# Optimization experiments

Measured on AMD Instinct MI355X. Metric: run time of the kernel, lower is better.

## Reference

```python
import jax, jax.numpy as jnp
import numpy as np

N_PARTICLES = 3_000_000
N_CVS = 30_000
N_MODELS = 8
FEATS = [64, 64, 64, 64]
E0, E1 = 2.0, 3.0
LN_EPS = 1e-5


def _dihedral(p):
    # p: [4,3] -> scalar dihedral angle (standard atan2 formulation)
    b1 = p[1] - p[0]
    b2 = p[2] - p[1]
    b3 = p[3] - p[2]
    n1 = jnp.cross(b1, b2)
    n2 = jnp.cross(b2, b3)
    m1 = jnp.cross(n1, b2 / jnp.linalg.norm(b2))
    return jnp.arctan2(jnp.dot(m1, n2), jnp.dot(n1, n2))


def _ensemble_energy(cvs, gamma, beta, Ws, bs):
    # cvs: [n_cvs] -> energy per model: [n_models]
    x = jnp.concatenate([jnp.cos(cvs), jnp.sin(cvs)])  # [2*n_cvs]
    mu = jnp.mean(x)
    var = jnp.mean((x - mu) ** 2)
    x = (x - mu) / jnp.sqrt(var + LN_EPS) * gamma + beta  # LayerNorm
    h = x[None, None, :]  # [1,1,2n] broadcasts against [M,2n,f]
    for i in range(len(Ws) - 1):
        h = jax.nn.relu(jnp.matmul(h, Ws[i]) + bs[i])  # [M,1,f]
    h = jnp.matmul(h, Ws[-1]) + bs[-1]  # [M,1,1]
    return h[:, 0, 0]  # [M]  (squeeze(-1) then batch dim 1)


def _uncertainty_weight(model_div):
    iswitch = (E1 - model_div) / (E1 - E0)
    fl = jnp.floor(iswitch)
    smooth = 0.5 * (1.0 + jnp.cos(jnp.pi * (1.0 - iswitch)))
    # heaviside(floor(iswitch), smooth): 1 if floor>0, smooth if floor==0, 0 if floor<0
    return jnp.where(fl > 0, 1.0, jnp.where(fl < 0, 0.0, smooth)).astype(model_div.dtype)


def setup_inputs() -> dict:
    key = jax.random.key(0)
    ks = jax.random.split(key, 16)
    positions = jax.random.normal(ks[0], (N_PARTICLES, 3), jnp.float32) * 3.0
    boxvectors = jnp.diag(jnp.full((3,), 10.0, dtype=jnp.float32))
    colvar_idx = jax.random.randint(ks[1], (N_CVS, 4), 0, N_PARTICLES)
    dims = [2 * N_CVS] + FEATS + [1]
    inp = {"positions": positions, "boxvectors": boxvectors, "colvar_idx": colvar_idx,
           "gamma": jnp.ones((2 * N_CVS,), jnp.float32),
           "beta": jnp.zeros((2 * N_CVS,), jnp.float32)}
    for i in range(5):
        bound = 1.0 / np.sqrt(dims[i])  # kaiming_uniform-like bound
        inp[f"W{i}"] = jax.random.uniform(ks[2 + i], (N_MODELS, dims[i], dims[i + 1]),
                                           jnp.float32, -bound, bound)
        inp[f"b{i}"] = jnp.zeros((N_MODELS, 1, dims[i + 1]), jnp.float32)
    return inp


def reference(positions, boxvectors, colvar_idx, gamma, beta,
              W0, b0, W1, b1, W2, b2, W3, b3, W4, b4):
    Ws = [W0, W1, W2, W3, W4]
    bs = [b0, b1, b2, b3, b4]
    boxsize = jnp.diag(boxvectors)  # [3]
    pos = positions - jnp.floor(positions / boxsize) * boxsize  # PBC wrap
    quads = pos[colvar_idx.reshape(-1)].reshape(-1, 4, 3)  # [n_cvs,4,3]
    cvs, dcvs_dx = jax.vmap(jax.value_and_grad(_dihedral))(quads)  # [n],[n,4,3]

    efn = lambda c: _ensemble_energy(c, gamma, beta, Ws, bs)  # [M]
    energy = efn(cvs)  # [M]
    mean_forces = -jax.jacrev(efn)(cvs)  # [M, n_cvs]: grad of -energy[m] wrt cvs

    model_div = jnp.sqrt(jnp.mean(jnp.var(mean_forces, axis=0, ddof=1)))
    sigma = _uncertainty_weight(model_div)
    mf = jnp.mean(mean_forces, axis=0)  # [n_cvs]
    contrib = (mf[:, None, None] * dcvs_dx).reshape(-1, 3)  # [n_cvs*4,3]
    forces = jnp.zeros_like(pos).at[colvar_idx.reshape(-1)].add(contrib)
    return energy.mean() * sigma, forces * sigma
```

## Files before the change

kernel.cpp:

```cpp
#include <hip/hip_runtime.h>
#include <math.h>

#define NCV   30000
#define NX    60000
#define NM    8
#define LN_EPSF 1e-5f
#define NFORCE 9000000

#define NB_CV 512
#define JB    59
#define NBX   235
#define NB_MF 118

#define WS_XRAW   0
#define WS_DCV    60000
#define WS_G      420000
#define WS_LNP    900000
#define WS_Z0P    901024
#define WS_DZ0    931232
#define WS_E      931744
#define WS_SGP    931752
#define WS_SGXP   933632
#define WS_VARSUM 935512
#define WS_TICKET 935513
#define WS_SIGMA  935514
#define WS_FLAG   935515

struct F3 { float x, y, z; };
__device__ __forceinline__ F3 f3sub(F3 a, F3 b){ return {a.x-b.x, a.y-b.y, a.z-b.z}; }
__device__ __forceinline__ F3 f3add(F3 a, F3 b){ return {a.x+b.x, a.y+b.y, a.z+b.z}; }
__device__ __forceinline__ F3 f3scale(F3 a, float s){ return {a.x*s, a.y*s, a.z*s}; }
__device__ __forceinline__ float f3dot(F3 a, F3 b){ return a.x*b.x + a.y*b.y + a.z*b.z; }
__device__ __forceinline__ F3 f3cross(F3 a, F3 b){
  return { a.y*b.z - a.z*b.y, a.z*b.x - a.x*b.z, a.x*b.y - a.y*b.x };
}

__device__ __forceinline__ void compute_mu_inv(const float* __restrict__ ws, float* out2, int tid) {
  if (tid < 64) {
    float a = 0.f, b = 0.f;
    #pragma unroll 4
    for (int k = tid; k < NB_CV; k += 64) { a += ws[WS_LNP + k]; b += ws[WS_LNP + NB_CV + k]; }
    #pragma unroll
    for (int o = 1; o < 64; o <<= 1) { a += __shfl_xor(a, o); b += __shfl_xor(b, o); }
    if (tid == 0) {
      float mu  = a * (1.f / NX);
      float var = b * (1.f / NX) - mu * mu;
      out2[0] = mu;
      out2[1] = 1.f / sqrtf(var + LN_EPSF);
    }
  }
}

__global__ void k_cv(const float* __restrict__ pos, const float* __restrict__ box,
                     const int* __restrict__ idx, float* __restrict__ ws) {
  int tid = threadIdx.x;
  int gtid = blockIdx.x * 256 + tid;
  if (gtid == 0) {
    ws[WS_VARSUM] = 0.f;
    ((unsigned int*)ws)[WS_TICKET] = 0u;
    ((unsigned int*)ws)[WS_FLAG]   = 0u;
  }

  float cx = 0.f, cx2 = 0.f;
  int i = gtid;
  if (i < NCV) {
    float bx = box[0], by = box[4], bz = box[8];
    int4 q4 = *(const int4*)(idx + i*4);
    int pidx[4] = {q4.x, q4.y, q4.z, q4.w};
    F3 p[4];
    #pragma unroll
    for (int a = 0; a < 4; a++) {
      int pi = pidx[a];
      float X = pos[(size_t)pi*3 + 0];
      float Y = pos[(size_t)pi*3 + 1];
      float Z = pos[(size_t)pi*3 + 2];
      X -= floorf(X / bx) * bx;
      Y -= floorf(Y / by) * by;
      Z -= floorf(Z / bz) * bz;
      p[a] = {X, Y, Z};
    }
    F3 b1 = f3sub(p[1], p[0]);
    F3 b2 = f3sub(p[2], p[1]);
    F3 b3 = f3sub(p[3], p[2]);
    F3 n1 = f3cross(b1, b2);
    F3 n2 = f3cross(b2, b3);
    float L = sqrtf(f3dot(b2, b2));
    F3 u = f3scale(b2, 1.f / L);
    F3 m1 = f3cross(n1, u);
    float yv = f3dot(m1, n2);
    float xv = f3dot(n1, n2);
    float h = sqrtf(xv*xv + yv*yv);
    float cphi = xv / h;
    float sphi = yv / h;

    float invd = 1.f / (h*h);
    float dX = -yv * invd;
    float dY =  xv * invd;
    F3 dn1 = f3scale(n2, dX);
    F3 dn2 = f3scale(n1, dX);
    F3 dm1 = f3scale(n2, dY);
    dn2 = f3add(dn2, f3scale(m1, dY));
    dn1 = f3add(dn1, f3cross(u, dm1));
    F3 du = f3cross(dm1, n1);
    float ud = f3dot(u, du);
    F3 db2 = f3scale(f3sub(du, f3scale(u, ud)), 1.f / L);
    db2 = f3add(db2, f3cross(b3, dn2));
    F3 db3 = f3cross(dn2, b2);
    F3 db1 = f3cross(b2, dn1);
    db2 = f3add(db2, f3cross(dn1, b1));

    F3 g0 = f3scale(db1, -1.f);
    F3 g1 = f3sub(db1, db2);
    F3 g2 = f3sub(db2, db3);
    F3 g3 = db3;

    ws[WS_XRAW + i]       = cphi;
    ws[WS_XRAW + NCV + i] = sphi;
    float* dc = ws + WS_DCV + (size_t)i * 12;
    dc[0] = g0.x; dc[1]  = g0.y; dc[2]  = g0.z;
    dc[3] = g1.x; dc[4]  = g1.y; dc[5]  = g1.z;
    dc[6] = g2.x; dc[7]  = g2.y; dc[8]  = g2.z;
    dc[9] = g3.x; dc[10] = g3.y; dc[11] = g3.z;

    cx  = cphi + sphi;
    cx2 = cphi*cphi + sphi*sphi;
  }

  #pragma unroll
  for (int o = 1; o < 64; o <<= 1) { cx += __shfl_xor(cx, o); cx2 += __shfl_xor(cx2, o); }
  __shared__ float sa[4], sb[4];
  int w = tid >> 6, l = tid & 63;
  if (l == 0) { sa[w] = cx; sb[w] = cx2; }
  __syncthreads();
  if (tid == 0) {
    ws[WS_LNP + blockIdx.x]         = sa[0] + sa[1] + sa[2] + sa[3];
    ws[WS_LNP + NB_CV + blockIdx.x] = sb[0] + sb[1] + sb[2] + sb[3];
  }
}

__global__ void k_z0(const float4* __restrict__ W0, const float* __restrict__ gamma,
                     const float* __restrict__ beta, float* __restrict__ ws,
                     float* __restrict__ out) {
  __shared__ float stats[2];
  __shared__ float yl[1024];
  __shared__ float red[4][16][4];
  int tid = threadIdx.x;
  int jb = blockIdx.x, m = blockIdx.y;
  int j0 = jb * 1024;
  int jcount = min(1024, NX - j0);

  {
    int gtid = (m * JB + jb) * 256 + tid;
    float4 z4 = {0.f, 0.f, 0.f, 0.f};
    float4* fz = (float4*)(out + 4);
    const int NF4 = (NFORCE - 4) / 4;
    for (int i = gtid; i < NF4; i += JB * NM * 256) fz[i] = z4;
    if (gtid == 0) { out[1] = 0.f; out[2] = 0.f; out[3] = 0.f; out[NFORCE] = 0.f; }
  }

  compute_mu_inv(ws, stats, tid);
  __syncthreads();
  float mu = stats[0], inv = stats[1];
  for (int jj = tid; jj < 1024; jj += 256) {
    int gj = j0 + jj;
    yl[jj] = (gj < NX) ? ((ws[WS_XRAW + gj] - mu) * inv * gamma[gj] + beta[gj]) : 0.f;
  }
  __syncthreads();

  int k4 = tid & 15;
  int r  = tid >> 4;
  const float4* Wm = W0 + (size_t)m * NX * 16;
  float4 acc = {0.f, 0.f, 0.f, 0.f};
  #pragma unroll 4
  for (int j = r; j < jcount; j += 16) {
    float y = yl[j];
    float4 wv = Wm[(size_t)(j0 + j) * 16 + k4];
    acc.x += y * wv.x; acc.y += y * wv.y; acc.z += y * wv.z; acc.w += y * wv.w;
  }
  #pragma unroll
  for (int o = 16; o <= 32; o <<= 1) {
    acc.x += __shfl_xor(acc.x, o); acc.y += __shfl_xor(acc.y, o);
    acc.z += __shfl_xor(acc.z, o); acc.w += __shfl_xor(acc.w, o);
  }
  int w = tid >> 6, l = tid & 63;
  if (l < 16) {
    red[w][l][0] = acc.x; red[w][l][1] = acc.y; red[w][l][2] = acc.z; red[w][l][3] = acc.w;
  }
  __syncthreads();
  if (tid < 64) {
    int kk4 = tid & 15, c = tid >> 4;
    float v = red[0][kk4][c] + red[1][kk4][c] + red[2][kk4][c] + red[3][kk4][c];
    ws[WS_Z0P + ((size_t)m * JB + jb) * 64 + kk4 * 4 + c] = v;
  }
}

__global__ void k_mlp(const float* __restrict__ ws_ro, const float* __restrict__ b0,
                      const float* __restrict__ W1, const float* __restrict__ b1,
                      const float* __restrict__ W2, const float* __restrict__ b2,
                      const float* __restrict__ W3, const float* __restrict__ b3,
                      const float* __restrict__ W4, const float* __restrict__ b4,
                      float* __restrict__ ws) {
  int m = blockIdx.x;
  int tid = threadIdx.x;
  int k = tid & 63, q = tid >> 6;
  __shared__ float Wl[3][64*65];
  __shared__ float hs[4][64];
  __shared__ float part[256];
  __shared__ float ds[64];

  const float* Wsrc0 = W1 + m*4096;
  const float* Wsrc1 = W2 + m*4096;
  const float* Wsrc2 = W3 + m*4096;
  for (int e = tid; e < 4096; e += 256) {
    int t = e >> 6, kk = e & 63;
    Wl[0][t*65 + kk] = Wsrc0[e];
    Wl[1][t*65 + kk] = Wsrc1[e];
    Wl[2][t*65 + kk] = Wsrc2[e];
  }

  float p0 = 0.f;
  for (int jb = q; jb < JB; jb += 4)
    p0 += ws_ro[WS_Z0P + ((size_t)m * JB + jb) * 64 + k];
  part[tid] = p0;
  __syncthreads();
  if (tid < 64) {
    float a0 = b0[m*64 + k] + part[k] + part[64+k] + part[128+k] + part[192+k];
    hs[0][k] = fmaxf(a0, 0.f);
  }
  __syncthreads();

  #pragma unroll
  for (int l = 0; l < 3; l++) {
    float pp = 0.f;
    #pragma unroll
    for (int t0 = 0; t0 < 16; t0++) {
      int t = q*16 + t0;
      pp += hs[l][t] * Wl[l][t*65 + k];
    }
    part[tid] = pp;
    __syncthreads();
    if (tid < 64) {
      const float* bl = (l==0) ? b1 : (l==1) ? b2 : b3;
      float a = bl[m*64+k] + part[k] + part[64+k] + part[128+k] + part[192+k];
      hs[l+1][k] = fmaxf(a, 0.f);
    }
    __syncthreads();
  }

  if (tid < 64) {
    float w4k = W4[m*64 + k];
    float e = hs[3][k] * w4k;
    #pragma unroll
    for (int o = 1; o < 64; o <<= 1) e += __shfl_xor(e, o);
    if (k == 0) ws[WS_E + m] = e + b4[m];
    ds[k] = (hs[3][k] > 0.f) ? w4k : 0.f;
  }
  __syncthreads();

  #pragma unroll
  for (int l = 2; l >= 0; l--) {
    float pp = 0.f;
    int t = k;
    #pragma unroll
    for (int k0 = 0; k0 < 16; k0++) {
      int kk = q*16 + k0;
      pp += Wl[l][t*65 + kk] * ds[kk];
    }
    part[tid] = pp;
    __syncthreads();
    if (tid < 64) {
      float dh = part[k] + part[64+k] + part[128+k] + part[192+k];
      float dz = (hs[l][k] > 0.f) ? dh : 0.f;
      if (l == 0) ws[WS_DZ0 + m*64 + k] = dz;
      else        ds[k] = dz;
    }
    __syncthreads();
  }
}

__global__ void k_bwdx(const float4* __restrict__ W0, const float* __restrict__ gamma,
                       float* __restrict__ ws) {
  __shared__ float stats[2];
  __shared__ float dz[64];
  __shared__ float sa[4], sb[4];
  int tid = threadIdx.x;
  int m = blockIdx.y, blk = blockIdx.x;

  compute_mu_inv(ws, stats, tid);
  if (tid >= 64 && tid < 128) dz[tid - 64] = ws[WS_DZ0 + m*64 + (tid - 64)];
  __syncthreads();
  float mu = stats[0], inv = stats[1];

  int c = tid & 15;
  int g = tid >> 4;
  const float4* dz4 = (const float4*)dz;
  float4 d4 = dz4[c];

  float sg = 0.f, sgx = 0.f;
  #pragma unroll 2
  for (int it = 0; it < 16; it++) {
    int j = blk * 256 + it * 16 + g;
    if (j < NX) {
      float4 wv = W0[((size_t)m * NX + j) * 16 + c];
      float dot = wv.x*d4.x + wv.y*d4.y + wv.z*d4.z + wv.w*d4.w;
      #pragma unroll
      for (int o = 1; o < 16; o <<= 1) dot += __shfl_xor(dot, o);
      if (c == 0) {
        float gg = dot * gamma[j];
        ws[WS_G + (size_t)m * NX + j] = gg;
        float xh = (ws[WS_XRAW + j] - mu) * inv;
        sg += gg; sgx += gg * xh;
      }
    }
  }
  #pragma unroll
  for (int o = 1; o < 64; o <<= 1) { sg += __shfl_xor(sg, o); sgx += __shfl_xor(sgx, o); }
  int w = tid >> 6, l = tid & 63;
  if (l == 0) { sa[w] = sg; sb[w] = sgx; }
  __syncthreads();
  if (tid == 0) {
    ws[WS_SGP  + m * NBX + blk] = sa[0] + sa[1] + sa[2] + sa[3];
    ws[WS_SGXP + m * NBX + blk] = sb[0] + sb[1] + sb[2] + sb[3];
  }
}

__global__ void k_mf(const int* __restrict__ idx, float* __restrict__ ws,
                     float* __restrict__ out) {
  __shared__ float stats[2];
  __shared__ float sSg[NM], sSgx[NM];
  __shared__ float sv[4];
  __shared__ float ssig;
  int tid = threadIdx.x;
  int w = tid >> 6, l = tid & 63;

  compute_mu_inv(ws, stats, tid);
  for (int m = w; m < NM; m += 4) {
    float a = 0.f, b = 0.f;
    #pragma unroll 2
    for (int bb = l; bb < NBX; bb += 64) { a += ws[WS_SGP + m*NBX + bb]; b += ws[WS_SGXP + m*NBX + bb]; }
    #pragma unroll
    for (int o = 1; o < 64; o <<= 1) { a += __shfl_xor(a, o); b += __shfl_xor(b, o); }
    if (l == 0) { sSg[m] = a * (1.f / NX); sSgx[m] = b * (1.f / NX); }
  }
  __syncthreads();
  float mu = stats[0], inv = stats[1];

  int i = blockIdx.x * 256 + tid;
  float v = 0.f, fm = 0.f;
  if (i < NCV) {
    float cph = ws[WS_XRAW + i], sph = ws[WS_XRAW + NCV + i];
    float xc = (cph - mu) * inv, xs = (sph - mu) * inv;
    float f[NM];
    #pragma unroll
    for (int m = 0; m < NM; m++) {
      float gc = ws[WS_G + (size_t)m * NX + i];
      float gs = ws[WS_G + (size_t)m * NX + NCV + i];
      float dxc = inv * (gc - sSg[m] - xc * sSgx[m]);
      float dxs = inv * (gs - sSg[m] - xs * sSgx[m]);
      float dE = dxc * (-sph) + dxs * cph;
      f[m] = -dE;
      fm += f[m];
    }
    fm *= (1.f / NM);
    float acc = 0.f;
    #pragma unroll
    for (int m = 0; m < NM; m++) { float d = f[m] - fm; acc += d * d; }
    v = acc * (1.f / (NM - 1));
  }
  #pragma unroll
  for (int o = 1; o < 64; o <<= 1) v += __shfl_xor(v, o);
  if (l == 0) sv[w] = v;
  __syncthreads();
  if (tid == 0) {
    atomicAdd(&ws[WS_VARSUM], sv[0] + sv[1] + sv[2] + sv[3]);
    __threadfence();
    unsigned int* tick = (unsigned int*)ws + WS_TICKET;
    unsigned int old = atomicAdd(tick, 1u);
    if (old == NB_MF - 1) {
      float tot = atomicAdd(&ws[WS_VARSUM], 0.0f);
      float md = sqrtf(tot * (1.f / NCV));
      float isw = (3.0f - md) / (3.0f - 2.0f);
      float fl = floorf(isw);
      float smooth = 0.5f * (1.f + cosf(3.14159265358979323846f * (1.f - isw)));
      float sigma = (fl > 0.f) ? 1.f : ((fl < 0.f) ? 0.f : smooth);
      float em = 0.f;
      #pragma unroll
      for (int m = 0; m < NM; m++) em += ws[WS_E + m];
      em *= (1.f / NM);
      out[0] = em * sigma;
      __hip_atomic_store(ws + WS_SIGMA, sigma, __ATOMIC_RELAXED, __HIP_MEMORY_SCOPE_AGENT);
      __hip_atomic_store((unsigned int*)ws + WS_FLAG, 1u, __ATOMIC_RELEASE, __HIP_MEMORY_SCOPE_AGENT);
    }
    while (__hip_atomic_load((unsigned int*)ws + WS_FLAG, __ATOMIC_ACQUIRE,
                             __HIP_MEMORY_SCOPE_AGENT) == 0u) {
      __builtin_amdgcn_s_sleep(8);
    }
    ssig = __hip_atomic_load(ws + WS_SIGMA, __ATOMIC_RELAXED, __HIP_MEMORY_SCOPE_AGENT);
  }
  __syncthreads();
  float sigma = ssig;

  if (i < NCV) {
    const float* dc = ws + WS_DCV + (size_t)i * 12;
    float4 d0 = *(const float4*)(dc);
    float4 d1 = *(const float4*)(dc + 4);
    float4 d2 = *(const float4*)(dc + 8);
    int4 q4 = *(const int4*)(idx + i*4);
    float s = fm * sigma;
    float* fp = out + 1;
    atomicAdd(&fp[(size_t)q4.x*3 + 0], s*d0.x);
    atomicAdd(&fp[(size_t)q4.x*3 + 1], s*d0.y);
    atomicAdd(&fp[(size_t)q4.x*3 + 2], s*d0.z);
    atomicAdd(&fp[(size_t)q4.y*3 + 0], s*d0.w);
    atomicAdd(&fp[(size_t)q4.y*3 + 1], s*d1.x);
    atomicAdd(&fp[(size_t)q4.y*3 + 2], s*d1.y);
    atomicAdd(&fp[(size_t)q4.z*3 + 0], s*d1.z);
    atomicAdd(&fp[(size_t)q4.z*3 + 1], s*d1.w);
    atomicAdd(&fp[(size_t)q4.z*3 + 2], s*d2.x);
    atomicAdd(&fp[(size_t)q4.w*3 + 0], s*d2.y);
    atomicAdd(&fp[(size_t)q4.w*3 + 1], s*d2.z);
    atomicAdd(&fp[(size_t)q4.w*3 + 2], s*d2.w);
  }
}

extern "C" void kernel_launch(void* const* d_in, const int* in_sizes, int n_in,
                              void* d_out, int out_size, void* d_ws, size_t ws_size,
                              hipStream_t stream) {
  const float* pos   = (const float*)d_in[0];
  const float* box   = (const float*)d_in[1];
  const int*   idx   = (const int*)  d_in[2];
  const float* gamma = (const float*)d_in[3];
  const float* beta  = (const float*)d_in[4];
  const float* W0 = (const float*)d_in[5];
  const float* b0 = (const float*)d_in[6];
  const float* W1 = (const float*)d_in[7];
  const float* b1 = (const float*)d_in[8];
  const float* W2 = (const float*)d_in[9];
  const float* b2 = (const float*)d_in[10];
  const float* W3 = (const float*)d_in[11];
  const float* b3 = (const float*)d_in[12];
  const float* W4 = (const float*)d_in[13];
  const float* b4 = (const float*)d_in[14];
  float* ws  = (float*)d_ws;
  float* out = (float*)d_out;

  k_cv<<<NB_CV, 256, 0, stream>>>(pos, box, idx, ws);
  k_z0<<<dim3(JB, NM), 256, 0, stream>>>((const float4*)W0, gamma, beta, ws, out);
  k_mlp<<<NM, 256, 0, stream>>>(ws, b0, W1, b1, W2, b2, W3, b3, W4, b4, ws);
  k_bwdx<<<dim3(NBX, NM), 256, 0, stream>>>((const float4*)W0, gamma, ws);
  k_mf<<<NB_MF, 256, 0, stream>>>(idx, ws, out);
}
```

Before: 100.7 us.

## Split W0 projection into finer blocks, move force zeroing, use SoA gradients

Shrinks each k_z0 block to 128 rows so the W0 projection runs on many more blocks. The force-buffer zeroing moves from k_z0 into k_cv. The dihedral gradient storage changes to a structure-of-arrays layout for coalesced stores and loads. k_bwdx batches four W0 loads before the reductions to raise memory-level parallelism. In exchange, k_mlp must reduce eight times more partial sums, and k_cv now carries the large zeroing write.

```diff
diff --git a/kernel.cpp b/kernel.cpp
--- a/kernel.cpp
+++ b/kernel.cpp
@@ -8,7 +8,7 @@
 #define NFORCE 9000000
 
 #define NB_CV 512
-#define JB    59
+#define JB    469
 #define NBX   235
 #define NB_MF 118
 
@@ -17,14 +17,14 @@
 #define WS_G      420000
 #define WS_LNP    900000
 #define WS_Z0P    901024
-#define WS_DZ0    931232
-#define WS_E      931744
-#define WS_SGP    931752
-#define WS_SGXP   933632
-#define WS_VARSUM 935512
-#define WS_TICKET 935513
-#define WS_SIGMA  935514
-#define WS_FLAG   935515
+#define WS_DZ0    1141152
+#define WS_E      1141664
+#define WS_SGP    1141672
+#define WS_SGXP   1143552
+#define WS_VARSUM 1145432
+#define WS_TICKET 1145433
+#define WS_SIGMA  1145434
+#define WS_FLAG   1145435
 
 struct F3 { float x, y, z; };
 __device__ __forceinline__ F3 f3sub(F3 a, F3 b){ return {a.x-b.x, a.y-b.y, a.z-b.z}; }
@@ -52,13 +52,22 @@
 }
 
 __global__ void k_cv(const float* __restrict__ pos, const float* __restrict__ box,
-                     const int* __restrict__ idx, float* __restrict__ ws) {
+                     const int* __restrict__ idx, float* __restrict__ ws,
+                     float* __restrict__ out) {
   int tid = threadIdx.x;
   int gtid = blockIdx.x * 256 + tid;
-  if (gtid == 0) {
-    ws[WS_VARSUM] = 0.f;
-    ((unsigned int*)ws)[WS_TICKET] = 0u;
-    ((unsigned int*)ws)[WS_FLAG]   = 0u;
+
+  {
+    float4 z4 = {0.f, 0.f, 0.f, 0.f};
+    float4* fz = (float4*)(out + 4);
+    const int NF4 = (NFORCE - 4) / 4;
+    for (int i = gtid; i < NF4; i += NB_CV * 256) fz[i] = z4;
+    if (gtid == 0) {
+      out[1] = 0.f; out[2] = 0.f; out[3] = 0.f; out[NFORCE] = 0.f;
+      ws[WS_VARSUM] = 0.f;
+      ((unsigned int*)ws)[WS_TICKET] = 0u;
+      ((unsigned int*)ws)[WS_FLAG]   = 0u;
+    }
   }
 
   float cx = 0.f, cx2 = 0.f;
@@ -116,11 +125,10 @@
 
     ws[WS_XRAW + i]       = cphi;
     ws[WS_XRAW + NCV + i] = sphi;
-    float* dc = ws + WS_DCV + (size_t)i * 12;
-    dc[0] = g0.x; dc[1]  = g0.y; dc[2]  = g0.z;
-    dc[3] = g1.x; dc[4]  = g1.y; dc[5]  = g1.z;
-    dc[6] = g2.x; dc[7]  = g2.y; dc[8]  = g2.z;
-    dc[9] = g3.x; dc[10] = g3.y; dc[11] = g3.z;
+    ws[WS_DCV + 0*NCV  + i] = g0.x; ws[WS_DCV + 1*NCV  + i] = g0.y; ws[WS_DCV + 2*NCV  + i] = g0.z;
+    ws[WS_DCV + 3*NCV  + i] = g1.x; ws[WS_DCV + 4*NCV  + i] = g1.y; ws[WS_DCV + 5*NCV  + i] = g1.z;
+    ws[WS_DCV + 6*NCV  + i] = g2.x; ws[WS_DCV + 7*NCV  + i] = g2.y; ws[WS_DCV + 8*NCV  + i] = g2.z;
+    ws[WS_DCV + 9*NCV  + i] = g3.x; ws[WS_DCV + 10*NCV + i] = g3.y; ws[WS_DCV + 11*NCV + i] = g3.z;
 
     cx  = cphi + sphi;
     cx2 = cphi*cphi + sphi*sphi;
@@ -139,31 +147,21 @@
 }
 
 __global__ void k_z0(const float4* __restrict__ W0, const float* __restrict__ gamma,
-                     const float* __restrict__ beta, float* __restrict__ ws,
-                     float* __restrict__ out) {
+                     const float* __restrict__ beta, float* __restrict__ ws) {
   __shared__ float stats[2];
-  __shared__ float yl[1024];
+  __shared__ float yl[128];
   __shared__ float red[4][16][4];
   int tid = threadIdx.x;
   int jb = blockIdx.x, m = blockIdx.y;
-  int j0 = jb * 1024;
-  int jcount = min(1024, NX - j0);
-
-  {
-    int gtid = (m * JB + jb) * 256 + tid;
-    float4 z4 = {0.f, 0.f, 0.f, 0.f};
-    float4* fz = (float4*)(out + 4);
-    const int NF4 = (NFORCE - 4) / 4;
-    for (int i = gtid; i < NF4; i += JB * NM * 256) fz[i] = z4;
-    if (gtid == 0) { out[1] = 0.f; out[2] = 0.f; out[3] = 0.f; out[NFORCE] = 0.f; }
-  }
+  int j0 = jb * 128;
+  int jcount = min(128, NX - j0);
 
   compute_mu_inv(ws, stats, tid);
   __syncthreads();
   float mu = stats[0], inv = stats[1];
-  for (int jj = tid; jj < 1024; jj += 256) {
-    int gj = j0 + jj;
-    yl[jj] = (gj < NX) ? ((ws[WS_XRAW + gj] - mu) * inv * gamma[gj] + beta[gj]) : 0.f;
+  if (tid < 128) {
+    int gj = j0 + tid;
+    yl[tid] = (gj < NX) ? ((ws[WS_XRAW + gj] - mu) * inv * gamma[gj] + beta[gj]) : 0.f;
   }
   __syncthreads();
 
@@ -171,11 +169,14 @@
   int r  = tid >> 4;
   const float4* Wm = W0 + (size_t)m * NX * 16;
   float4 acc = {0.f, 0.f, 0.f, 0.f};
-  #pragma unroll 4
-  for (int j = r; j < jcount; j += 16) {
-    float y = yl[j];
-    float4 wv = Wm[(size_t)(j0 + j) * 16 + k4];
-    acc.x += y * wv.x; acc.y += y * wv.y; acc.z += y * wv.z; acc.w += y * wv.w;
+  #pragma unroll
+  for (int it = 0; it < 8; it++) {
+    int j = it * 16 + r;
+    if (j < jcount) {
+      float y = yl[j];
+      float4 wv = Wm[(size_t)(j0 + j) * 16 + k4];
+      acc.x += y * wv.x; acc.y += y * wv.y; acc.z += y * wv.z; acc.w += y * wv.w;
+    }
   }
   #pragma unroll
   for (int o = 16; o <= 32; o <<= 1) {
@@ -297,15 +298,23 @@
   float4 d4 = dz4[c];
 
   float sg = 0.f, sgx = 0.f;
-  #pragma unroll 2
-  for (int it = 0; it < 16; it++) {
-    int j = blk * 256 + it * 16 + g;
-    if (j < NX) {
-      float4 wv = W0[((size_t)m * NX + j) * 16 + c];
-      float dot = wv.x*d4.x + wv.y*d4.y + wv.z*d4.z + wv.w*d4.w;
+  #pragma unroll
+  for (int it = 0; it < 4; it++) {
+    int jbase = blk * 256 + it * 64 + g;
+    float4 wv[4];
+    #pragma unroll
+    for (int u = 0; u < 4; u++) {
+      int j = jbase + u * 16;
+      if (j < NX) wv[u] = W0[((size_t)m * NX + j) * 16 + c];
+      else        wv[u] = {0.f, 0.f, 0.f, 0.f};
+    }
+    #pragma unroll
+    for (int u = 0; u < 4; u++) {
+      int j = jbase + u * 16;
+      float dot = wv[u].x*d4.x + wv[u].y*d4.y + wv[u].z*d4.z + wv[u].w*d4.w;
       #pragma unroll
       for (int o = 1; o < 16; o <<= 1) dot += __shfl_xor(dot, o);
-      if (c == 0) {
+      if (c == 0 && j < NX) {
         float gg = dot * gamma[j];
         ws[WS_G + (size_t)m * NX + j] = gg;
         float xh = (ws[WS_XRAW + j] - mu) * inv;
@@ -401,25 +410,24 @@
   float sigma = ssig;
 
   if (i < NCV) {
-    const float* dc = ws + WS_DCV + (size_t)i * 12;
-    float4 d0 = *(const float4*)(dc);
-    float4 d1 = *(const float4*)(dc + 4);
-    float4 d2 = *(const float4*)(dc + 8);
+    float d[12];
+    #pragma unroll
+    for (int r = 0; r < 12; r++) d[r] = ws[WS_DCV + r*NCV + i];
     int4 q4 = *(const int4*)(idx + i*4);
     float s = fm * sigma;
     float* fp = out + 1;
-    atomicAdd(&fp[(size_t)q4.x*3 + 0], s*d0.x);
-    atomicAdd(&fp[(size_t)q4.x*3 + 1], s*d0.y);
-    atomicAdd(&fp[(size_t)q4.x*3 + 2], s*d0.z);
-    atomicAdd(&fp[(size_t)q4.y*3 + 0], s*d0.w);
-    atomicAdd(&fp[(size_t)q4.y*3 + 1], s*d1.x);
-    atomicAdd(&fp[(size_t)q4.y*3 + 2], s*d1.y);
-    atomicAdd(&fp[(size_t)q4.z*3 + 0], s*d1.z);
-    atomicAdd(&fp[(size_t)q4.z*3 + 1], s*d1.w);
-    atomicAdd(&fp[(size_t)q4.z*3 + 2], s*d2.x);
-    atomicAdd(&fp[(size_t)q4.w*3 + 0], s*d2.y);
-    atomicAdd(&fp[(size_t)q4.w*3 + 1], s*d2.z);
-    atomicAdd(&fp[(size_t)q4.w*3 + 2], s*d2.w);
+    atomicAdd(&fp[(size_t)q4.x*3 + 0], s*d[0]);
+    atomicAdd(&fp[(size_t)q4.x*3 + 1], s*d[1]);
+    atomicAdd(&fp[(size_t)q4.x*3 + 2], s*d[2]);
+    atomicAdd(&fp[(size_t)q4.y*3 + 0], s*d[3]);
+    atomicAdd(&fp[(size_t)q4.y*3 + 1], s*d[4]);
+    atomicAdd(&fp[(size_t)q4.y*3 + 2], s*d[5]);
+    atomicAdd(&fp[(size_t)q4.z*3 + 0], s*d[6]);
+    atomicAdd(&fp[(size_t)q4.z*3 + 1], s*d[7]);
+    atomicAdd(&fp[(size_t)q4.z*3 + 2], s*d[8]);
+    atomicAdd(&fp[(size_t)q4.w*3 + 0], s*d[9]);
+    atomicAdd(&fp[(size_t)q4.w*3 + 1], s*d[10]);
+    atomicAdd(&fp[(size_t)q4.w*3 + 2], s*d[11]);
   }
 }
 
@@ -444,8 +452,8 @@
   float* ws  = (float*)d_ws;
   float* out = (float*)d_out;
 
-  k_cv<<<NB_CV, 256, 0, stream>>>(pos, box, idx, ws);
-  k_z0<<<dim3(JB, NM), 256, 0, stream>>>((const float4*)W0, gamma, beta, ws, out);
+  k_cv<<<NB_CV, 256, 0, stream>>>(pos, box, idx, ws, out);
+  k_z0<<<dim3(JB, NM), 256, 0, stream>>>((const float4*)W0, gamma, beta, ws);
   k_mlp<<<NM, 256, 0, stream>>>(ws, b0, W1, b1, W2, b2, W3, b3, W4, b4, ws);
   k_bwdx<<<dim3(NBX, NM), 256, 0, stream>>>((const float4*)W0, gamma, ws);
   k_mf<<<NB_MF, 256, 0, stream>>>(idx, ws, out);
```

Result: slower. 127.2 us (+26.4%).
